# Kernel tuning notes

Measured on AMD Instinct MI355X. Metric: run time of the kernel, lower is better.

Reference implementation:

```python
import jax, jax.numpy as jnp
import numpy as np

B, L, S, H, E, D = 2, 2048, 2048, 16, 64, 64

def setup_inputs() -> dict:
    key = jax.random.key(0)
    kq, kk, kv = jax.random.split(key, 3)
    queries = jax.random.normal(kq, (B, L, H, E), dtype=jnp.float32)
    keys = jax.random.normal(kk, (B, S, H, E), dtype=jnp.float32)
    values = jax.random.normal(kv, (B, S, H, D), dtype=jnp.float32)
    # TriangularCausalMask: True above the diagonal (masked positions)
    causal = jnp.triu(jnp.ones((L, S), dtype=bool), k=1)
    attn_mask = jnp.broadcast_to(causal[None, None], (B, 1, L, S))
    z = jnp.zeros((1,), dtype=jnp.float32)
    return {"queries": queries, "keys": keys, "values": values,
            "query_omegas": z, "query_thetas": z, "key_omegas": z,
            "key_thetas": z, "attn_mask": attn_mask}

def reference(queries, keys, values, query_omegas, query_thetas,
              key_omegas, key_thetas, attn_mask):
    # omegas/thetas are unused in FullAttention.forward (kept for signature parity)
    scale = 1.0 / jnp.sqrt(jnp.float32(E))
    scores = jnp.einsum('blhe,bshe->bhls', queries, keys)  # [B,H,L,S]
    scores = jnp.where(attn_mask, -jnp.inf, scores)
    A = jax.nn.softmax(scale * scores, axis=-1)  # dropout p=0 (eval)
    V = jnp.einsum('bhls,bshd->blhd', A, values)
    return V
```

## Files before the change

kernel.cpp:

```cpp
#include <hip/hip_runtime.h>
#include <hip/hip_bf16.h>
#include <math.h>

typedef __attribute__((ext_vector_type(8))) short bf16x8;
typedef __attribute__((ext_vector_type(16))) float f32x16;

#define B_ 2
#define L_ 2048
#define S_ 2048
#define H_ 16
#define E_ 64
#define D_ 64

__device__ __forceinline__ float exp2fast(float x) {
  float r;
  asm("v_exp_f32 %0, %1" : "=v"(r) : "v"(x));
  return r;
}
#define EXP2(x) exp2fast(x)

#define KOFF 0ull
#define VOFF (8ull << 20)
#define POFF (16ull << 20)
#define SLOT_BYTES 18432ull
#define NSLOTS 1120ull
#define WS_NEED (POFF + NSLOTS * SLOT_BYTES)

#define GLL(gp, lp) __builtin_amdgcn_global_load_lds( \
    (const __attribute__((address_space(1))) unsigned int*)(gp), \
    (__attribute__((address_space(3))) unsigned int*)(lp), 16, 0, 0)

__device__ __forceinline__ unsigned pkbf(float a, float b) {
  __hip_bfloat162 hh = __float22bfloat162_rn(float2{a, b});
  return *(unsigned*)&hh;
}
__device__ __forceinline__ float bf2f(unsigned us) {
  return __uint_as_float(us << 16);
}
__device__ __forceinline__ int crow(int r, int hi5) {
  return (r & 3) + ((r >> 2) << 3) + (hi5 << 2);
}
__device__ __forceinline__ int nchunks(int q) { return (q >= 10) ? 3 : ((q >= 3) ? 2 : 1); }
__device__ __forceinline__ int slotoff(int q, int c) {
  return (q < 3) ? q : (q < 10) ? 3 + (q - 3) * 2 + c : 17 + (q - 10) * 3 + c;
}

__global__ __launch_bounds__(256)
void fa_pre(const float* __restrict__ Kp, const float* __restrict__ Vp,
            char* __restrict__ ws) {
  const int Bx = blockIdx.x;
  const int bh = Bx & 31, t = Bx >> 5;
  const int b = bh >> 4, h = bh & 15;
  const int kv0 = t * 64;
  const int tid = threadIdx.x;
  char* dk = ws + KOFF + ((size_t)(bh * 32 + t)) * 8192;
  char* dv = ws + VOFF + ((size_t)(bh * 32 + t)) * 8192;
  const int krow = tid >> 2, ksg = tid & 3;
  const int kswz = (krow & 7) << 4;
  const float* gk = Kp + ((size_t)(b * S_ + kv0 + krow) * H_ + h) * E_ + ksg * 16;
  float4 a0 = ((const float4*)gk)[0], a1 = ((const float4*)gk)[1];
  float4 a2 = ((const float4*)gk)[2], a3 = ((const float4*)gk)[3];
  uint4 u0{pkbf(a0.x, a0.y), pkbf(a0.z, a0.w), pkbf(a1.x, a1.y), pkbf(a1.z, a1.w)};
  uint4 u1{pkbf(a2.x, a2.y), pkbf(a2.z, a2.w), pkbf(a3.x, a3.y), pkbf(a3.z, a3.w)};
  *(uint4*)(dk + ((krow * 128 + ksg * 32) ^ kswz)) = u0;
  *(uint4*)(dk + ((krow * 128 + ksg * 32 + 16) ^ kswz)) = u1;
  const int vd = tid & 63, kg = tid >> 6;
  const int vswz = (vd & 7) << 4;
  const float* gv = Vp + ((size_t)(b * S_ + kv0 + kg * 16) * H_ + h) * D_ + vd;
  float v[16];
  #pragma unroll
  for (int k = 0; k < 16; ++k) v[k] = gv[(size_t)k * (H_ * D_)];
  uint4 w0{pkbf(v[0], v[1]), pkbf(v[2], v[3]), pkbf(v[4], v[5]), pkbf(v[6], v[7])};
  uint4 w1{pkbf(v[8], v[9]), pkbf(v[10], v[11]), pkbf(v[12], v[13]), pkbf(v[14], v[15])};
  *(uint4*)(dv + ((vd * 128 + kg * 32) ^ vswz)) = w0;
  *(uint4*)(dv + ((vd * 128 + kg * 32 + 16) ^ vswz)) = w1;
}

__global__ __launch_bounds__(256, 4)
void fa_main(const float* __restrict__ Qp, float* __restrict__ Op,
             char* __restrict__ ws) {
  __shared__ uint4 sbuf[2][1024];

  const int tid  = threadIdx.x;
  const int lane = tid & 63;
  const int sub  = tid >> 6;
  const int l31  = lane & 31;
  const int hi5  = lane >> 5;

  const int Bx  = blockIdx.x;
  const int xcd = Bx & 7, i_ = Bx >> 3;
  const int bh  = xcd * 4 + (i_ & 3);
  const int j   = i_ >> 2;
  int q, c;
  if (j < 18)      { q = 15 - j / 3;       c = j % 3; }
  else if (j < 32) { q = 9 - (j - 18) / 2; c = (j - 18) & 1; }
  else             { q = 34 - j;           c = 0; }
  const int b = bh >> 4, h = bh & 15;
  const int tot = 2 * q + 2, nc = nchunks(q);
  const int base = tot / nc, rem = tot - base * nc;
  const int R  = base + (c < rem ? 1 : 0);
  const int t0 = c * base + (c < rem ? c : rem);
  const int q0 = q << 7;
  const int qw = q0 + sub * 32;

  const float cs = 0.125f * 1.44269504088896f;

  bf16x8 qf[4];
  {
    const int qg = qw + l31;
    const float* gq = Qp + ((size_t)(b * L_ + qg) * H_ + h) * E_ + hi5 * 8;
    #pragma unroll
    for (int ec = 0; ec < 4; ++ec) {
      float4 a = *(const float4*)(gq + ec * 16);
      float4 cc = *(const float4*)(gq + ec * 16 + 4);
      uint4 u;
      u.x = pkbf(a.x * cs, a.y * cs);
      u.y = pkbf(a.z * cs, a.w * cs);
      u.z = pkbf(cc.x * cs, cc.y * cs);
      u.w = pkbf(cc.z * cs, cc.w * cs);
      qf[ec] = *(bf16x8*)&u;
    }
  }

  f32x16 acc[2];
  #pragma unroll
  for (int dt = 0; dt < 2; ++dt)
    #pragma unroll
    for (int rr = 0; rr < 16; ++rr) acc[dt][rr] = 0.f;
  float mrun = -INFINITY, lsum = 0.f;

  const char* gK = ws + KOFF + ((size_t)bh * 32) * 8192;
  const char* gV = ws + VOFF + ((size_t)bh * 32) * 8192;

#define STAGE(buf_, t_) do {                                        \
    const char* sk = gK + (size_t)(t_) * 8192 + tid * 16;           \
    const char* sv = gV + (size_t)(t_) * 8192 + tid * 16;           \
    char* lb = (char*)&sbuf[(buf_)][0] + tid * 16;                  \
    GLL(sk, lb); GLL(sk + 4096, lb + 4096);                         \
    GLL(sv, lb + 8192); GLL(sv + 4096, lb + 12288);                 \
  } while (0)

  STAGE(0, t0);
  __syncthreads();

  int cur = 0;
  for (int t = t0; t < t0 + R; ++t, cur ^= 1) {
    if (t + 1 < t0 + R) STAGE(cur ^ 1, t + 1);

    const int kv0 = t * 64;
    if (kv0 <= qw + 31) {
      char* lk = (char*)&sbuf[cur][0];
      char* lv = lk + 8192;
      const bool needmask = (kv0 + 63) > qw;

      f32x16 st[2];
      #pragma unroll
      for (int c2 = 0; c2 < 2; ++c2)
        #pragma unroll
        for (int rr = 0; rr < 16; ++rr) st[c2][rr] = 0.f;
      __builtin_amdgcn_s_setprio(1);
      #pragma unroll
      for (int c2 = 0; c2 < 2; ++c2) {
        const int row = c2 * 32 + l31;
        const int sw = (row & 7) << 4;
        #pragma unroll
        for (int ec = 0; ec < 4; ++ec) {
          bf16x8 kf = *(bf16x8*)(lk + ((row * 128 + ec * 32 + hi5 * 16) ^ sw));
          st[c2] = __builtin_amdgcn_mfma_f32_32x32x16_bf16(kf, qf[ec], st[c2], 0, 0, 0);
        }
      }
      __builtin_amdgcn_s_setprio(0);

      if (needmask) {
        const int qg = qw + l31;
        #pragma unroll
        for (int c2 = 0; c2 < 2; ++c2)
          #pragma unroll
          for (int rr = 0; rr < 16; ++rr)
            if (kv0 + c2 * 32 + crow(rr, hi5) > qg) st[c2][rr] = -1e30f;
      }

      float mx[8];
      #pragma unroll
      for (int i = 0; i < 8; ++i)
        mx[i] = fmaxf(fmaxf(st[0][i], st[0][i + 8]),
                      fmaxf(st[1][i], st[1][i + 8]));
      #pragma unroll
      for (int i = 0; i < 4; ++i) mx[i] = fmaxf(mx[i], mx[i + 4]);
      mx[0] = fmaxf(mx[0], mx[2]);
      mx[1] = fmaxf(mx[1], mx[3]);
      float pm = fmaxf(mx[0], mx[1]);
      pm = fmaxf(pm, __shfl_xor(pm, 32));

      if (__any(pm > mrun + 8.f)) {
        const float mn = fmaxf(mrun, pm);
        const float f = EXP2(mrun - mn);
        mrun = mn;
        lsum *= f;
        #pragma unroll
        for (int rr = 0; rr < 16; ++rr) {
          const float fr = __shfl(f, crow(rr, hi5));
          acc[0][rr] *= fr;
          acc[1][rr] *= fr;
        }
      }
      {
        #pragma unroll
        for (int c2 = 0; c2 < 2; ++c2)
          #pragma unroll
          for (int rr = 0; rr < 16; ++rr)
            st[c2][rr] = EXP2(st[c2][rr] - mrun);
        float ss[8];
        #pragma unroll
        for (int i = 0; i < 8; ++i)
          ss[i] = (st[0][i] + st[0][i + 8]) + (st[1][i] + st[1][i + 8]);
        #pragma unroll
        for (int i = 0; i < 4; ++i) ss[i] += ss[i + 4];
        float ps = (ss[0] + ss[2]) + (ss[1] + ss[3]);
        ps += __shfl_xor(ps, 32);
        lsum += ps;
      }

      uint4 pa[4];
      #pragma unroll
      for (int c2 = 0; c2 < 2; ++c2) {
        unsigned Dw[8];
        #pragma unroll
        for (int jj = 0; jj < 8; ++jj)
          Dw[jj] = pkbf(st[c2][2 * jj], st[c2][2 * jj + 1]);
        unsigned y0 = __shfl_xor((int)(hi5 ? Dw[0] : Dw[2]), 32);
        unsigned y1 = __shfl_xor((int)(hi5 ? Dw[1] : Dw[3]), 32);
        unsigned y2 = __shfl_xor((int)(hi5 ? Dw[4] : Dw[6]), 32);
        unsigned y3 = __shfl_xor((int)(hi5 ? Dw[5] : Dw[7]), 32);
        uint4 p0, p1;
        if (hi5) {
          p0 = uint4{y0, y1, Dw[2], Dw[3]};
          p1 = uint4{y2, y3, Dw[6], Dw[7]};
        } else {
          p0 = uint4{Dw[0], Dw[1], y0, y1};
          p1 = uint4{Dw[4], Dw[5], y2, y3};
        }
        pa[2 * c2]     = p0;
        pa[2 * c2 + 1] = p1;
      }

      __builtin_amdgcn_s_setprio(1);
      #pragma unroll
      for (int s = 0; s < 4; ++s) {
        #pragma unroll
        for (int dt = 0; dt < 2; ++dt) {
          const int row = dt * 32 + l31;
          bf16x8 vf = *(bf16x8*)(lv + ((row * 128 + s * 32 + hi5 * 16) ^ ((row & 7) << 4)));
          acc[dt] = __builtin_amdgcn_mfma_f32_32x32x16_bf16(*(bf16x8*)&pa[s], vf, acc[dt], 0, 0, 0);
        }
      }
      __builtin_amdgcn_s_setprio(0);
    }
    __syncthreads();
  }

  if (nc == 1) {
    const float inv = 1.f / lsum;
    #pragma unroll
    for (int rr = 0; rr < 16; ++rr) {
      const int cr = crow(rr, hi5);
      const float wv = __shfl(inv, cr);
      const int qg = qw + cr;
      float* go = Op + ((size_t)(b * L_ + qg) * H_ + h) * D_ + l31;
      go[0]  = acc[0][rr] * wv;
      go[32] = acc[1][rr] * wv;
    }
    return;
  }

  char* slot = ws + POFF + ((size_t)(bh * 35 + slotoff(q, c))) * SLOT_BYTES;
  uint4* pw = (uint4*)(slot + (size_t)(sub * 64 + lane) * 64);
  #pragma unroll
  for (int dt = 0; dt < 2; ++dt) {
    uint4 A{pkbf(acc[dt][0], acc[dt][1]),  pkbf(acc[dt][2], acc[dt][3]),
            pkbf(acc[dt][4], acc[dt][5]),  pkbf(acc[dt][6], acc[dt][7])};
    uint4 Bq{pkbf(acc[dt][8], acc[dt][9]),  pkbf(acc[dt][10], acc[dt][11]),
             pkbf(acc[dt][12], acc[dt][13]), pkbf(acc[dt][14], acc[dt][15])};
    pw[dt * 2]     = A;
    pw[dt * 2 + 1] = Bq;
  }
  ((float2*)(slot + 16384))[sub * 64 + lane] = float2{mrun, lsum};
#undef STAGE
}

__device__ __forceinline__ void unpk(uint4 a, uint4 b, float* o) {
  const unsigned* pa = (const unsigned*)&a;
  const unsigned* pb = (const unsigned*)&b;
  #pragma unroll
  for (int i = 0; i < 4; ++i) {
    o[2 * i]     = bf2f(pa[i] & 0xffffu);
    o[2 * i + 1] = bf2f(pa[i] >> 16);
    o[8 + 2 * i]     = bf2f(pb[i] & 0xffffu);
    o[8 + 2 * i + 1] = bf2f(pb[i] >> 16);
  }
}

__global__ __launch_bounds__(256)
void fa_merge(float* __restrict__ Op, const char* __restrict__ ws) {
  const int Bx = blockIdx.x;
  const int bh = Bx / 13, q = 3 + (Bx % 13);
  const int b = bh >> 4, h = bh & 15;
  const int tid = threadIdx.x, lane = tid & 63, sub = tid >> 6;
  const int l31 = lane & 31, hi5 = lane >> 5;
  const int nc = nchunks(q);
  const char* sbase = ws + POFF;

  float A0[16], A1[16], M, Lw;
  {
    const char* s0 = sbase + ((size_t)(bh * 35 + slotoff(q, 0))) * SLOT_BYTES;
    const uint4* pr = (const uint4*)(s0 + (size_t)(sub * 64 + lane) * 64);
    unpk(pr[0], pr[1], A0);
    unpk(pr[2], pr[3], A1);
    float2 ml = ((const float2*)(s0 + 16384))[sub * 64 + lane];
    M = ml.x; Lw = ml.y;
  }
  for (int ci = 1; ci < nc; ++ci) {
    const char* si = sbase + ((size_t)(bh * 35 + slotoff(q, ci))) * SLOT_BYTES;
    const uint4* pr = (const uint4*)(si + (size_t)(sub * 64 + lane) * 64);
    float a0[16], a1[16];
    unpk(pr[0], pr[1], a0);
    unpk(pr[2], pr[3], a1);
    float2 ml = ((const float2*)(si + 16384))[sub * 64 + lane];
    const float mm = fmaxf(M, ml.x);
    const float fA = EXP2(M - mm);
    const float fI = EXP2(ml.x - mm);
    Lw = Lw * fA + ml.y * fI;
    M = mm;
    #pragma unroll
    for (int rr = 0; rr < 16; ++rr) {
      const int cr = crow(rr, hi5);
      const float fAb = __shfl(fA, cr);
      const float fIb = __shfl(fI, cr);
      A0[rr] = A0[rr] * fAb + a0[rr] * fIb;
      A1[rr] = A1[rr] * fAb + a1[rr] * fIb;
    }
  }
  const float inv = 1.f / Lw;
  #pragma unroll
  for (int rr = 0; rr < 16; ++rr) {
    const int cr = crow(rr, hi5);
    const float wv = __shfl(inv, cr);
    const int qg = (q << 7) + sub * 32 + cr;
    float* go = Op + ((size_t)(b * L_ + qg) * H_ + h) * D_ + l31;
    go[0]  = A0[rr] * wv;
    go[32] = A1[rr] * wv;
  }
}

extern "C" void kernel_launch(void* const* d_in, const int* in_sizes, int n_in,
                              void* d_out, int out_size, void* d_ws, size_t ws_size,
                              hipStream_t stream) {
  (void)in_sizes; (void)n_in; (void)out_size; (void)ws_size;
  const float* Q = (const float*)d_in[0];
  const float* K = (const float*)d_in[1];
  const float* V = (const float*)d_in[2];
  float* O = (float*)d_out;
  char* ws = (char*)d_ws;
  fa_pre<<<dim3(1024), dim3(256), 0, stream>>>(K, V, ws);
  fa_main<<<dim3(1120), dim3(256), 0, stream>>>(Q, O, ws);
  fa_merge<<<dim3(416), dim3(256), 0, stream>>>(O, ws);
}
```

Before: 58.00 us.

## Fold max subtraction into MFMA accumulator init and use partial vmcnt barriers

The score accumulator is initialized to the negative running max, so the QK MFMA output already holds the shifted logits. This removes a per-element subtraction before exp2, and the running max starts at zero instead of -inf. The per-tile __syncthreads is replaced by explicit s_waitcnt vmcnt with s_barrier, so the current tile only waits for its own loads while the next tile's global-to-LDS loads stay in flight. This relies on the hand-counted vmcnt matching the number of issued loads and on correct ordering of LDS reuse. Starting the max at zero also changes the numerics for rows whose logits are all very negative.

```diff
diff --git a/kernel.cpp b/kernel.cpp
--- a/kernel.cpp
+++ b/kernel.cpp
@@ -127,7 +127,7 @@
   for (int dt = 0; dt < 2; ++dt)
     #pragma unroll
     for (int rr = 0; rr < 16; ++rr) acc[dt][rr] = 0.f;
-  float mrun = -INFINITY, lsum = 0.f;
+  float mrun = 0.f, lsum = 0.f;
 
   const char* gK = ws + KOFF + ((size_t)bh * 32) * 8192;
   const char* gV = ws + VOFF + ((size_t)bh * 32) * 8192;
@@ -141,11 +141,17 @@
   } while (0)
 
   STAGE(0, t0);
-  __syncthreads();
+  asm volatile("s_waitcnt vmcnt(0)\n\ts_barrier" ::: "memory");
 
   int cur = 0;
   for (int t = t0; t < t0 + R; ++t, cur ^= 1) {
-    if (t + 1 < t0 + R) STAGE(cur ^ 1, t + 1);
+    const bool have_next = (t + 1) < (t0 + R);
+    if (have_next) {
+      STAGE(cur ^ 1, t + 1);
+      asm volatile("s_waitcnt vmcnt(4)\n\ts_barrier" ::: "memory");
+    } else {
+      asm volatile("s_waitcnt vmcnt(0)\n\ts_barrier" ::: "memory");
+    }
 
     const int kv0 = t * 64;
     if (kv0 <= qw + 31) {
@@ -154,10 +160,11 @@
       const bool needmask = (kv0 + 63) > qw;
 
       f32x16 st[2];
+      const float nm = -mrun;
       #pragma unroll
       for (int c2 = 0; c2 < 2; ++c2)
         #pragma unroll
-        for (int rr = 0; rr < 16; ++rr) st[c2][rr] = 0.f;
+        for (int rr = 0; rr < 16; ++rr) st[c2][rr] = nm;
       __builtin_amdgcn_s_setprio(1);
       #pragma unroll
       for (int c2 = 0; c2 < 2; ++c2) {
@@ -189,13 +196,13 @@
       for (int i = 0; i < 4; ++i) mx[i] = fmaxf(mx[i], mx[i + 4]);
       mx[0] = fmaxf(mx[0], mx[2]);
       mx[1] = fmaxf(mx[1], mx[3]);
-      float pm = fmaxf(mx[0], mx[1]);
-      pm = fmaxf(pm, __shfl_xor(pm, 32));
-
-      if (__any(pm > mrun + 8.f)) {
-        const float mn = fmaxf(mrun, pm);
-        const float f = EXP2(mrun - mn);
-        mrun = mn;
+      float pmx = fmaxf(mx[0], mx[1]);
+      pmx = fmaxf(pmx, __shfl_xor(pmx, 32));
+
+      if (__any(pmx > 8.f)) {
+        pmx = fmaxf(pmx, 0.f);
+        const float f = EXP2(-pmx);
+        mrun += pmx;
         lsum *= f;
         #pragma unroll
         for (int rr = 0; rr < 16; ++rr) {
@@ -203,13 +210,18 @@
           acc[0][rr] *= fr;
           acc[1][rr] *= fr;
         }
+        const float npmx = -pmx;
+        #pragma unroll
+        for (int c2 = 0; c2 < 2; ++c2)
+          #pragma unroll
+          for (int rr = 0; rr < 16; ++rr) st[c2][rr] += npmx;
       }
       {
         #pragma unroll
         for (int c2 = 0; c2 < 2; ++c2)
           #pragma unroll
           for (int rr = 0; rr < 16; ++rr)
-            st[c2][rr] = EXP2(st[c2][rr] - mrun);
+            st[c2][rr] = EXP2(st[c2][rr]);
         float ss[8];
         #pragma unroll
         for (int i = 0; i < 8; ++i)
@@ -256,7 +268,7 @@
       }
       __builtin_amdgcn_s_setprio(0);
     }
-    __syncthreads();
+    asm volatile("s_barrier" ::: "memory");
   }
 
   if (nc == 1) {
```

Result: no change. 57.36 us (-1.1%).
